# Performance work log

Hardware: AMD Instinct MI355X
Metric: run time of the kernel (lower is better)

## Reference

```python
import jax, jax.numpy as jnp
import numpy as np

BINS = 128
H, W = 4096, 4096


def setup_inputs() -> dict:
    key = jax.random.key(0)
    k1, k2 = jax.random.split(key)
    img = jax.random.randint(k1, (H, W, 3), 0, 256, dtype=jnp.int32)
    mask = jax.random.uniform(k2, (H, W), dtype=jnp.float32)
    full = jnp.zeros((BINS, BINS, BINS), dtype=jnp.float32)
    lines = jnp.zeros((BINS, BINS, BINS), dtype=jnp.float32)
    return {"img": img, "mask": mask, "full": full, "lines": lines}


def reference(img, mask, full, lines):
    # quantize 0..255 -> 0..127 (matches uint8 img // 2)
    q = (img // 2)[:, :, :3]
    h, w, _ = q.shape
    flat = q.reshape(h * w, 3)  # [N, 3] bin indices
    r, g, b = flat[:, 0], flat[:, 1], flat[:, 2]

    # _push_image: scatter-add into 128^3 histograms
    full2 = full.at[r, g, b].add(1.0)
    lines2 = lines.at[r, g, b].add(mask.reshape(h * w))

    # get_ratios: normalized log-likelihood-ratio threshold filter
    l = lines2 + 1e-10
    f = full2 + 1.0
    l = l / jnp.sum(l)
    f = f / jnp.sum(f)
    log_ratios = jnp.log(l / f)
    avg_log_ratios = jnp.sum(l * log_ratios)
    color_filter = log_ratios > avg_log_ratios  # [128,128,128] bool

    # _apply_filter: per-pixel gather from the 3D lookup table
    out = color_filter[q[..., 0], q[..., 1], q[..., 2]]  # [H, W] bool
    return out
```

## Files before the change

### kernel.cpp

```cpp
#include <hip/hip_runtime.h>
#include <stdint.h>


typedef uint32_t u32x4 __attribute__((ext_vector_type(4)));

#define P1_BLK    512
#define P1_PIXG   1024

#define NBKT_N    128
#define SHIFT_N   14
#define CAP_N     135168
#define NBKT_M    512
#define SHIFT_M   12
#define CAP_M     34816
#define BPB_M     4096

#define NSUB      32
#define SUBCAP    4608
#define NSEG      (NBKT_N * NSUB)
#define P15_SPLIT 8

template<int NB, int SHIFT, int CAPV, bool WBPIX>
__global__ __launch_bounds__(P1_BLK) void p1_scatter_det(
    const u32x4* __restrict__ img4, const u32x4* __restrict__ mask4,
    uint32_t* __restrict__ cursor,
    unsigned short* __restrict__ gbin, unsigned long long* __restrict__ gpm,
    u32x4* __restrict__ bpix4)
{
    __shared__ uint32_t s_cnt[NB];
    __shared__ uint32_t s_start[NB];
    __shared__ int      s_adj[NB];
    __shared__ uint32_t s_wsum[P1_BLK / 64];
    __shared__ uint32_t s_bin[P1_PIXG * 4];
    __shared__ unsigned long long s_pm[P1_PIXG * 4];

    const int tid = threadIdx.x;
    if (tid < NB) s_cnt[tid] = 0;
    __syncthreads();

    const int g0 = blockIdx.x * P1_PIXG;
    uint32_t bin[8], rk[8];
    unsigned long long pm[8];

    #pragma unroll
    for (int k = 0; k < 2; ++k) {
        int g = g0 + tid + k * P1_BLK;
        u32x4 a = __builtin_nontemporal_load(&img4[3 * g + 0]);
        u32x4 b = __builtin_nontemporal_load(&img4[3 * g + 1]);
        u32x4 c = __builtin_nontemporal_load(&img4[3 * g + 2]);
        u32x4 m = __builtin_nontemporal_load(&mask4[g]);
        uint32_t b0 = ((a.x >> 1) << 14) | ((a.y >> 1) << 7) | (a.z >> 1);
        uint32_t b1 = ((a.w >> 1) << 14) | ((b.x >> 1) << 7) | (b.y >> 1);
        uint32_t b2 = ((b.z >> 1) << 14) | ((b.w >> 1) << 7) | (c.x >> 1);
        uint32_t b3 = ((c.y >> 1) << 14) | ((c.z >> 1) << 7) | (c.w >> 1);
        if (WBPIX) {
            u32x4 bb = {b0, b1, b2, b3};
            __builtin_nontemporal_store(bb, &bpix4[g]);
        }
        unsigned long long p0 = (unsigned long long)(4u * (uint32_t)g);
        bin[4*k+0] = b0; pm[4*k+0] = ((p0 + 0) << 32) | m.x; rk[4*k+0] = atomicAdd(&s_cnt[b0 >> SHIFT], 1u);
        bin[4*k+1] = b1; pm[4*k+1] = ((p0 + 1) << 32) | m.y; rk[4*k+1] = atomicAdd(&s_cnt[b1 >> SHIFT], 1u);
        bin[4*k+2] = b2; pm[4*k+2] = ((p0 + 2) << 32) | m.z; rk[4*k+2] = atomicAdd(&s_cnt[b2 >> SHIFT], 1u);
        bin[4*k+3] = b3; pm[4*k+3] = ((p0 + 3) << 32) | m.w; rk[4*k+3] = atomicAdd(&s_cnt[b3 >> SHIFT], 1u);
    }
    __syncthreads();

    uint32_t v = (tid < NB) ? s_cnt[tid] : 0u;
    uint32_t inc = v;
    #pragma unroll
    for (int o = 1; o < 64; o <<= 1) {
        uint32_t n = __shfl_up(inc, o, 64);
        if ((tid & 63) >= o) inc += n;
    }
    if ((tid & 63) == 63) s_wsum[tid >> 6] = inc;
    __syncthreads();
    if (tid == 0) {
        uint32_t run = 0;
        #pragma unroll
        for (int w = 0; w < P1_BLK / 64; ++w) { uint32_t t = s_wsum[w]; s_wsum[w] = run; run += t; }
    }
    __syncthreads();
    uint32_t start = inc - v + s_wsum[tid >> 6];
    if (tid < NB) {
        s_start[tid] = start;
        uint32_t gb = v ? atomicAdd(&cursor[tid], v) : 0u;
        s_adj[tid] = (int)gb - (int)start;
    }
    __syncthreads();

    #pragma unroll
    for (int k = 0; k < 8; ++k) {
        uint32_t slot = s_start[bin[k] >> SHIFT] + rk[k];
        s_bin[slot] = bin[k];
        s_pm[slot]  = pm[k];
    }
    __syncthreads();

    for (int i = tid; i < P1_PIXG * 4; i += P1_BLK) {
        uint32_t bf = s_bin[i];
        uint32_t bk = bf >> SHIFT;
        uint32_t pos = (uint32_t)(s_adj[bk] + i);
        if (pos < (uint32_t)CAPV) {
            size_t idx = (size_t)bk * CAPV + pos;
            gbin[idx] = (unsigned short)(bf & ((1u << SHIFT) - 1u));
            gpm[idx]  = s_pm[i];
        }
    }
}

__global__ __launch_bounds__(1024) void p15_subpart(
    const unsigned short* __restrict__ gbin,
    const unsigned long long* __restrict__ gpm,
    const uint32_t* __restrict__ cursor,
    unsigned short* __restrict__ gb2,
    unsigned long long* __restrict__ gpm2,
    uint32_t* __restrict__ cnt2)
{
    __shared__ uint32_t s_c[NSUB], s_st[NSUB + 1], s_gp[NSUB];
    __shared__ unsigned short s_sb[4096];
    __shared__ unsigned long long s_sp[4096];

    const int tid  = threadIdx.x;
    const int b    = blockIdx.x >> 3;
    const int part = blockIdx.x & (P15_SPLIT - 1);
    uint32_t n = cursor[b];
    if (n > CAP_N) n = CAP_N;
    const size_t base = (size_t)b * CAP_N;

    for (uint32_t c0 = (uint32_t)part * 4096u; c0 < n; c0 += P15_SPLIT * 4096u) {
        const uint32_t cn = (n - c0 < 4096u) ? (n - c0) : 4096u;
        if (tid < NSUB) s_c[tid] = 0u;
        __syncthreads();

        uint32_t myb[4]; unsigned long long myp[4]; uint32_t myr[4];
        #pragma unroll
        for (int k = 0; k < 4; ++k) {
            uint32_t i = (uint32_t)tid + k * 1024u;
            if (i < cn) {
                uint32_t bl = gbin[base + c0 + i];
                myp[k] = gpm[base + c0 + i];
                myr[k] = atomicAdd(&s_c[bl >> 9], 1u);
                myb[k] = bl;
            } else myb[k] = 0xFFFFFFFFu;
        }
        __syncthreads();
        if (tid == 0) {
            uint32_t run = 0;
            #pragma unroll
            for (int r = 0; r < NSUB; ++r) { s_st[r] = run; run += s_c[r]; }
            s_st[NSUB] = run;
        }
        if (tid < NSUB) {
            uint32_t c = s_c[tid];
            s_gp[tid] = c ? atomicAdd(&cnt2[b * NSUB + tid], c) : 0u;
        }
        __syncthreads();
        #pragma unroll
        for (int k = 0; k < 4; ++k) {
            if (myb[k] != 0xFFFFFFFFu) {
                uint32_t slot = s_st[myb[k] >> 9] + myr[k];
                s_sb[slot] = (unsigned short)myb[k];
                s_sp[slot] = myp[k];
            }
        }
        __syncthreads();

        for (uint32_t i = tid; i < cn; i += 1024) {
            uint32_t bl = s_sb[i];
            uint32_t r = bl >> 9;
            uint32_t pos = s_gp[r] + (i - s_st[r]);
            if (pos < SUBCAP) {
                size_t d = ((size_t)b * NSUB + r) * SUBCAP + pos;
                gb2[d]  = (unsigned short)bl;
                gpm2[d] = s_sp[i];
            }
        }
        __syncthreads();
    }
}

__global__ __launch_bounds__(512) void p2_binhist(
    const unsigned short* __restrict__ gb2,
    const unsigned long long* __restrict__ gpm2,
    const uint32_t* __restrict__ cnt2,
    uint32_t* __restrict__ counts, float* __restrict__ lsum)
{
    __shared__ uint32_t s_cnt[512], s_start[512];
    __shared__ uint32_t s_wt[8];
    __shared__ unsigned long long s_srt[SUBCAP];

    const int tid = threadIdx.x;
    const int s = blockIdx.x;
    uint32_t n = cnt2[s];
    if (n > SUBCAP) n = SUBCAP;
    const size_t base = (size_t)s * SUBCAP;

    s_cnt[tid] = 0u;
    __syncthreads();

    uint32_t           myb[9];
    unsigned long long myp[9];
    uint32_t           myr[9];
    #pragma unroll
    for (int k = 0; k < 9; ++k) {
        uint32_t i = (uint32_t)tid + (uint32_t)k * 512u;
        if (i < n) {
            uint32_t lo = gb2[base + i] & 511u;
            myp[k] = gpm2[base + i];
            myr[k] = atomicAdd(&s_cnt[lo], 1u);
            myb[k] = lo;
        } else myb[k] = 0xFFFFFFFFu;
    }
    __syncthreads();

    uint32_t v = s_cnt[tid], inc = v;
    #pragma unroll
    for (int o = 1; o < 64; o <<= 1) {
        uint32_t t = __shfl_up(inc, o, 64);
        if ((tid & 63) >= o) inc += t;
    }
    if ((tid & 63) == 63) s_wt[tid >> 6] = inc;
    __syncthreads();
    if (tid == 0) {
        uint32_t run = 0;
        #pragma unroll
        for (int w = 0; w < 8; ++w) { uint32_t t = s_wt[w]; s_wt[w] = run; run += t; }
    }
    __syncthreads();
    const uint32_t st = s_wt[tid >> 6] + inc - v;
    s_start[tid] = st;
    __syncthreads();

    #pragma unroll
    for (int k = 0; k < 9; ++k) {
        if (myb[k] != 0xFFFFFFFFu)
            s_srt[s_start[myb[k]] + myr[k]] = myp[k];
    }
    __syncthreads();

    const uint32_t c = v;
    for (uint32_t x = 1; x < c; ++x) {
        unsigned long long val = s_srt[st + x];
        int y = (int)x - 1;
        while (y >= 0 && s_srt[st + y] > val) { s_srt[st + y + 1] = s_srt[st + y]; --y; }
        s_srt[st + y + 1] = val;
    }
    float sum = 0.0f;
    for (uint32_t x = 0; x < c; ++x)
        sum += __uint_as_float((uint32_t)s_srt[st + x]);
    counts[(size_t)s * 512 + tid] = c;
    lsum[(size_t)s * 512 + tid]   = sum;
}

__global__ __launch_bounds__(1024) void p2_sort_hist(
    const unsigned short* __restrict__ gbin,
    const unsigned long long* __restrict__ gpm,
    const uint32_t* __restrict__ cursor,
    unsigned long long* __restrict__ srt,
    uint32_t* __restrict__ counts, float* __restrict__ lsum)
{
    __shared__ uint32_t s_cnt[BPB_M];
    __shared__ uint32_t s_start[BPB_M];
    __shared__ uint32_t s_fill[BPB_M];
    __shared__ uint32_t s_wt[16];

    const int tid = threadIdx.x;
    const int b = blockIdx.x;
    for (int j = tid; j < BPB_M; j += 1024) s_cnt[j] = 0u;
    __syncthreads();

    uint32_t n = cursor[b];
    if (n > CAP_M) n = CAP_M;
    const size_t base = (size_t)b * CAP_M;

    for (uint32_t i = tid; i < n; i += 1024)
        atomicAdd(&s_cnt[gbin[base + i]], 1u);
    __syncthreads();

    const int j0 = tid * 4;
    uint32_t a0 = s_cnt[j0+0], a1 = s_cnt[j0+1], a2 = s_cnt[j0+2], a3 = s_cnt[j0+3];
    uint32_t s = a0 + a1 + a2 + a3;
    uint32_t inc = s;
    #pragma unroll
    for (int o = 1; o < 64; o <<= 1) {
        uint32_t t = __shfl_up(inc, o, 64);
        if ((tid & 63) >= o) inc += t;
    }
    if ((tid & 63) == 63) s_wt[tid >> 6] = inc;
    __syncthreads();
    if (tid == 0) {
        uint32_t run = 0;
        #pragma unroll
        for (int w = 0; w < 16; ++w) { uint32_t t = s_wt[w]; s_wt[w] = run; run += t; }
    }
    __syncthreads();
    uint32_t ex = s_wt[tid >> 6] + (inc - s);
    uint32_t e0 = ex, e1 = ex + a0, e2 = e1 + a1, e3 = e2 + a2;
    s_start[j0+0] = e0; s_start[j0+1] = e1; s_start[j0+2] = e2; s_start[j0+3] = e3;
    s_fill[j0+0] = 0u;  s_fill[j0+1] = 0u;  s_fill[j0+2] = 0u;  s_fill[j0+3] = 0u;
    __syncthreads();

    for (uint32_t i = tid; i < n; i += 1024) {
        uint32_t lo = gbin[base + i];
        unsigned long long pmv = __builtin_nontemporal_load(&gpm[base + i]);
        uint32_t slot = s_start[lo] + atomicAdd(&s_fill[lo], 1u);
        srt[base + slot] = pmv;
    }
    __threadfence_block();
    __syncthreads();

    uint32_t cs[4] = {a0, a1, a2, a3};
    uint32_t ss[4] = {e0, e1, e2, e3};
    #pragma unroll
    for (int t = 0; t < 4; ++t) {
        uint32_t c = cs[t];
        unsigned long long* arr = srt + base + ss[t];
        for (uint32_t x = 1; x < c; ++x) {
            unsigned long long v2 = arr[x];
            int y = (int)x - 1;
            while (y >= 0 && arr[y] > v2) { arr[y+1] = arr[y]; --y; }
            arr[y+1] = v2;
        }
        float sum = 0.0f;
        for (uint32_t x = 0; x < c; ++x)
            sum += __uint_as_float((uint32_t)arr[x]);
        size_t gbidx = (size_t)b * BPB_M + (size_t)(j0 + t);
        counts[gbidx] = c;
        lsum[gbidx]   = sum;
    }
}

__global__ void hist_direct_kernel(const u32x4* __restrict__ img4,
                                   const u32x4* __restrict__ mask4,
                                   uint32_t* __restrict__ counts,
                                   float* __restrict__ lsum, int npix4) {
    int t = blockIdx.x * blockDim.x + threadIdx.x;
    if (t >= npix4) return;
    u32x4 a = img4[3 * t + 0];
    u32x4 b = img4[3 * t + 1];
    u32x4 c = img4[3 * t + 2];
    u32x4 m = mask4[t];
    uint32_t b0 = ((a.x >> 1) << 14) | ((a.y >> 1) << 7) | (a.z >> 1);
    uint32_t b1 = ((a.w >> 1) << 14) | ((b.x >> 1) << 7) | (b.y >> 1);
    uint32_t b2 = ((b.z >> 1) << 14) | ((b.w >> 1) << 7) | (c.x >> 1);
    uint32_t b3 = ((c.y >> 1) << 14) | ((c.z >> 1) << 7) | (c.w >> 1);
    atomicAdd(&counts[b0], 1u);
    atomicAdd(&counts[b1], 1u);
    atomicAdd(&counts[b2], 1u);
    atomicAdd(&counts[b3], 1u);
    unsafeAtomicAdd(&lsum[b0], __uint_as_float(m.x));
    unsafeAtomicAdd(&lsum[b1], __uint_as_float(m.y));
    unsafeAtomicAdd(&lsum[b2], __uint_as_float(m.z));
    unsafeAtomicAdd(&lsum[b3], __uint_as_float(m.w));
}

__global__ __launch_bounds__(256) void reduce_lf_kernel(
    const uint32_t* __restrict__ counts, const float* __restrict__ lsum,
    const float* __restrict__ full_in, const float* __restrict__ lines_in,
    double* __restrict__ part_lf, int nbin) {
    double sl = 0.0, sf = 0.0;
    for (int i = blockIdx.x * 256 + threadIdx.x; i < nbin; i += 256 * 256) {
        float f = (float)counts[i] + full_in[i] + 1.0f;
        float l = (lsum[i] + lines_in[i]) + 1e-10f;
        sl += (double)l;
        sf += (double)f;
    }
    for (int o = 32; o > 0; o >>= 1) {
        sl += __shfl_down(sl, o, 64);
        sf += __shfl_down(sf, o, 64);
    }
    __shared__ double s0[4], s1[4];
    int lane = threadIdx.x & 63, wid = threadIdx.x >> 6;
    if (lane == 0) { s0[wid] = sl; s1[wid] = sf; }
    __syncthreads();
    if (threadIdx.x == 0) {
        part_lf[blockIdx.x * 2 + 0] = s0[0] + s0[1] + s0[2] + s0[3];
        part_lf[blockIdx.x * 2 + 1] = s1[0] + s1[1] + s1[2] + s1[3];
    }
}

__global__ void final_lf_kernel(const double* __restrict__ part_lf,
                                double* __restrict__ accum) {
    const int lane = threadIdx.x;
    double sl = 0.0, sf = 0.0;
    #pragma unroll
    for (int k = 0; k < 4; ++k) {
        sl += part_lf[2 * (lane + 64 * k) + 0];
        sf += part_lf[2 * (lane + 64 * k) + 1];
    }
    #pragma unroll
    for (int o = 32; o > 0; o >>= 1) {
        sl += __shfl_down(sl, o, 64);
        sf += __shfl_down(sf, o, 64);
    }
    if (lane == 0) { accum[0] = sl; accum[1] = sf; }
}

__global__ __launch_bounds__(256) void logr_kernel(
    const uint32_t* __restrict__ counts, const float* __restrict__ lsum,
    const float* __restrict__ full_in, const float* __restrict__ lines_in,
    const double* __restrict__ accum, double* __restrict__ part_avg,
    float* __restrict__ logr, int nbin) {
    float Sl = (float)accum[0];
    float Sf = (float)accum[1];
    double acc = 0.0;
    for (int i = blockIdx.x * 256 + threadIdx.x; i < nbin; i += 256 * 256) {
        float f = (float)counts[i] + full_in[i] + 1.0f;
        float l = (lsum[i] + lines_in[i]) + 1e-10f;
        float ln = l / Sl;
        float fn = f / Sf;
        float lr = logf(ln / fn);
        logr[i] = lr;
        acc += (double)(ln * lr);
    }
    for (int o = 32; o > 0; o >>= 1) acc += __shfl_down(acc, o, 64);
    __shared__ double s[4];
    int lane = threadIdx.x & 63, wid = threadIdx.x >> 6;
    if (lane == 0) s[wid] = acc;
    __syncthreads();
    if (threadIdx.x == 0) part_avg[blockIdx.x] = s[0] + s[1] + s[2] + s[3];
}

__global__ void final_avg_kernel(const double* __restrict__ part_avg,
                                 double* __restrict__ accum) {
    const int lane = threadIdx.x;
    double a = 0.0;
    #pragma unroll
    for (int k = 0; k < 4; ++k) a += part_avg[lane + 64 * k];
    #pragma unroll
    for (int o = 32; o > 0; o >>= 1) a += __shfl_down(a, o, 64);
    if (lane == 0) accum[2] = a;
}

__global__ void filt_kernel(const float* __restrict__ logr,
                            const double* __restrict__ accum,
                            unsigned long long* __restrict__ bits, int nbin) {
    float avg = (float)accum[2];
    int i = blockIdx.x * blockDim.x + threadIdx.x;
    bool p = (i < nbin) && (logr[i] > avg);
    unsigned long long m = __ballot(p);
    if ((threadIdx.x & 63) == 0 && i < nbin) bits[i >> 6] = m;
}

__global__ void out_kernel_bpix(const u32x4* __restrict__ bpix4,
                                const uint32_t* __restrict__ bits32,
                                u32x4* __restrict__ out4, int npix4) {
    int t = blockIdx.x * blockDim.x + threadIdx.x;
    if (t >= npix4) return;
    u32x4 b = __builtin_nontemporal_load(&bpix4[t]);
    u32x4 o = {(bits32[b.x >> 5] >> (b.x & 31u)) & 1u,
               (bits32[b.y >> 5] >> (b.y & 31u)) & 1u,
               (bits32[b.z >> 5] >> (b.z & 31u)) & 1u,
               (bits32[b.w >> 5] >> (b.w & 31u)) & 1u};
    __builtin_nontemporal_store(o, &out4[t]);
}

__global__ void out_kernel_img(const u32x4* __restrict__ img4,
                               const uint32_t* __restrict__ bits32,
                               u32x4* __restrict__ out4, int npix4) {
    int t = blockIdx.x * blockDim.x + threadIdx.x;
    if (t >= npix4) return;
    u32x4 a = __builtin_nontemporal_load(&img4[3 * t + 0]);
    u32x4 b = __builtin_nontemporal_load(&img4[3 * t + 1]);
    u32x4 c = __builtin_nontemporal_load(&img4[3 * t + 2]);
    uint32_t b0 = ((a.x >> 1) << 14) | ((a.y >> 1) << 7) | (a.z >> 1);
    uint32_t b1 = ((a.w >> 1) << 14) | ((b.x >> 1) << 7) | (b.y >> 1);
    uint32_t b2 = ((b.z >> 1) << 14) | ((b.w >> 1) << 7) | (c.x >> 1);
    uint32_t b3 = ((c.y >> 1) << 14) | ((c.z >> 1) << 7) | (c.w >> 1);
    u32x4 o = {(bits32[b0 >> 5] >> (b0 & 31u)) & 1u,
               (bits32[b1 >> 5] >> (b1 & 31u)) & 1u,
               (bits32[b2 >> 5] >> (b2 & 31u)) & 1u,
               (bits32[b3 >> 5] >> (b3 & 31u)) & 1u};
    __builtin_nontemporal_store(o, &out4[t]);
}

extern "C" void kernel_launch(void* const* d_in, const int* in_sizes, int n_in,
                              void* d_out, int out_size, void* d_ws, size_t ws_size,
                              hipStream_t stream) {
    const int*   img      = (const int*)d_in[0];
    const float* mask     = (const float*)d_in[1];
    const float* full_in  = (const float*)d_in[2];
    const float* lines_in = (const float*)d_in[3];

    const int npix  = in_sizes[1];
    const int nbin  = in_sizes[2];
    const int npix4 = npix / 4;

    char* ws = (char*)d_ws;
    const size_t ENT1 = (size_t)NBKT_M * CAP_M;
    const size_t ENT2 = (size_t)NSEG * SUBCAP;

    const size_t off_cursor = 64;
    const size_t off_plf    = off_cursor + 4ull * NBKT_M;
    const size_t off_pavg   = off_plf + 256ull * 2 * 8;
    const size_t off_cnt2   = off_pavg + 256ull * 8;
    const size_t off_hdrend = (off_cnt2 + 4ull * NSEG + 255ull) & ~255ull;
    const size_t off_counts = off_hdrend;
    const size_t off_lsum   = off_counts + 4ull * nbin;
    const size_t off_logr   = off_lsum + 4ull * nbin;
    const size_t off_filt   = off_logr + 4ull * nbin;
    const size_t off_gbin   = (off_filt + (size_t)nbin + 255ull) & ~255ull;
    const size_t off_gpm    = (off_gbin + 2ull * ENT1 + 255ull) & ~255ull;
    const size_t off_union  = off_gpm + 8ull * ENT1;
    const size_t need_mid   = off_union + 8ull * ENT1;
    const size_t off_gb2    = off_union;
    const size_t off_gpm2   = (off_gb2 + 2ull * ENT2 + 255ull) & ~255ull;
    const size_t need_new   = off_gpm2 + 8ull * ENT2;
    const size_t off_bpix   = (need_new + 255ull) & ~255ull;
    const size_t need_new2  = off_bpix + 4ull * (size_t)npix;

    double*   accum  = (double*)ws;
    uint32_t* cursor = (uint32_t*)(ws + off_cursor);
    double*   plf    = (double*)(ws + off_plf);
    double*   pavg   = (double*)(ws + off_pavg);
    uint32_t* cnt2   = (uint32_t*)(ws + off_cnt2);
    uint32_t* counts = (uint32_t*)(ws + off_counts);
    float*    lsum   = (float*)(ws + off_lsum);
    float*    logr   = (float*)(ws + off_logr);
    unsigned long long* fbits = (unsigned long long*)(ws + off_filt);
    const uint32_t*     fb32  = (const uint32_t*)(ws + off_filt);
    unsigned short*     gbin = (unsigned short*)(ws + off_gbin);
    unsigned long long* gpm  = (unsigned long long*)(ws + off_gpm);
    unsigned long long* srt  = (unsigned long long*)(ws + off_union);
    unsigned short*     gb2  = (unsigned short*)(ws + off_gb2);
    unsigned long long* gpm2 = (unsigned long long*)(ws + off_gpm2);
    u32x4*              bpix4 = (u32x4*)(ws + off_bpix);

    const bool shape_ok  = (nbin == NBKT_M * BPB_M) && (npix % (P1_PIXG * 4) == 0);
    const bool tier_new2 = shape_ok && ws_size >= need_new2;
    const bool tier_new  = shape_ok && ws_size >= need_new;
    const bool tier_mid  = shape_ok && ws_size >= need_mid;
    const int BLK = 256;

    if (tier_new2 || tier_new) {
        hipMemsetAsync(ws, 0, off_hdrend, stream);
        if (tier_new2) {
            p1_scatter_det<NBKT_N, SHIFT_N, CAP_N, true>
                <<<npix / (P1_PIXG * 4), P1_BLK, 0, stream>>>(
                (const u32x4*)img, (const u32x4*)mask, cursor, gbin, gpm, bpix4);
        } else {
            p1_scatter_det<NBKT_N, SHIFT_N, CAP_N, false>
                <<<npix / (P1_PIXG * 4), P1_BLK, 0, stream>>>(
                (const u32x4*)img, (const u32x4*)mask, cursor, gbin, gpm, nullptr);
        }
        p15_subpart<<<NBKT_N * P15_SPLIT, 1024, 0, stream>>>(
            gbin, gpm, cursor, gb2, gpm2, cnt2);
        p2_binhist<<<NSEG, 512, 0, stream>>>(gb2, gpm2, cnt2, counts, lsum);
    } else if (tier_mid) {
        hipMemsetAsync(ws, 0, off_hdrend, stream);
        p1_scatter_det<NBKT_M, SHIFT_M, CAP_M, false>
            <<<npix / (P1_PIXG * 4), P1_BLK, 0, stream>>>(
            (const u32x4*)img, (const u32x4*)mask, cursor, gbin, gpm, nullptr);
        p2_sort_hist<<<NBKT_M, 1024, 0, stream>>>(gbin, gpm, cursor, srt, counts, lsum);
    } else {
        hipMemsetAsync(ws, 0, off_logr, stream);
        hist_direct_kernel<<<(npix4 + BLK - 1) / BLK, BLK, 0, stream>>>(
            (const u32x4*)img, (const u32x4*)mask, counts, lsum, npix4);
    }

    reduce_lf_kernel<<<256, 256, 0, stream>>>(counts, lsum, full_in, lines_in, plf, nbin);
    final_lf_kernel<<<1, 64, 0, stream>>>(plf, accum);
    logr_kernel<<<256, 256, 0, stream>>>(counts, lsum, full_in, lines_in,
                                         accum, pavg, logr, nbin);
    final_avg_kernel<<<1, 64, 0, stream>>>(pavg, accum);
    filt_kernel<<<(nbin + BLK - 1) / BLK, BLK, 0, stream>>>(logr, accum, fbits, nbin);
    if (tier_new2) {
        out_kernel_bpix<<<(npix4 + BLK - 1) / BLK, BLK, 0, stream>>>(
            bpix4, fb32, (u32x4*)d_out, npix4);
    } else {
        out_kernel_img<<<(npix4 + BLK - 1) / BLK, BLK, 0, stream>>>(
            (const u32x4*)img, fb32, (u32x4*)d_out, npix4);
    }
}
```

Before: 690.0 us.

## Pack bin into 64-bit payload, fuse histogram finalize with l/f sum reduction

Drops the separate 16-bit bin array between the subpartition and per-bin histogram stages by packing the low bin bits, pixel index and 31-bit mask into one 64-bit word. The scatter stage stores a compact per-slot metadata word plus mask in shared memory instead of a 64-bit payload. The histogram kernel now computes the final f and l values and per-block partial sums directly, so the separate reduce pass over counts and lsum goes away. The cost is extra bit packing, a new constraint on pixel count, and extra fA/lA buffers.

```diff
diff --git a/kernel.cpp b/kernel.cpp
--- a/kernel.cpp
+++ b/kernel.cpp
@@ -20,27 +20,27 @@
 #define NSEG      (NBKT_N * NSUB)
 #define P15_SPLIT 8
 
-template<int NB, int SHIFT, int CAPV, bool WBPIX>
-__global__ __launch_bounds__(P1_BLK) void p1_scatter_det(
+template<bool WBPIX>
+__global__ __launch_bounds__(P1_BLK) void p1_scatter_new(
     const u32x4* __restrict__ img4, const u32x4* __restrict__ mask4,
     uint32_t* __restrict__ cursor,
     unsigned short* __restrict__ gbin, unsigned long long* __restrict__ gpm,
     u32x4* __restrict__ bpix4)
 {
-    __shared__ uint32_t s_cnt[NB];
-    __shared__ uint32_t s_start[NB];
-    __shared__ int      s_adj[NB];
+    __shared__ uint32_t s_cnt[NBKT_N];
+    __shared__ uint32_t s_start[NBKT_N];
+    __shared__ int      s_adj[NBKT_N];
     __shared__ uint32_t s_wsum[P1_BLK / 64];
-    __shared__ uint32_t s_bin[P1_PIXG * 4];
-    __shared__ unsigned long long s_pm[P1_PIXG * 4];
+    __shared__ uint32_t s_meta[P1_PIXG * 4];
+    __shared__ uint32_t s_msk[P1_PIXG * 4];
+    __shared__ uint8_t  s_bkt[P1_PIXG * 4];
 
     const int tid = threadIdx.x;
-    if (tid < NB) s_cnt[tid] = 0;
+    if (tid < NBKT_N) s_cnt[tid] = 0;
     __syncthreads();
 
     const int g0 = blockIdx.x * P1_PIXG;
-    uint32_t bin[8], rk[8];
-    unsigned long long pm[8];
+    uint32_t bin[8], rk[8], msk[8];
 
     #pragma unroll
     for (int k = 0; k < 2; ++k) {
@@ -57,6 +57,93 @@
             u32x4 bb = {b0, b1, b2, b3};
             __builtin_nontemporal_store(bb, &bpix4[g]);
         }
+        bin[4*k+0] = b0; msk[4*k+0] = m.x; rk[4*k+0] = atomicAdd(&s_cnt[b0 >> SHIFT_N], 1u);
+        bin[4*k+1] = b1; msk[4*k+1] = m.y; rk[4*k+1] = atomicAdd(&s_cnt[b1 >> SHIFT_N], 1u);
+        bin[4*k+2] = b2; msk[4*k+2] = m.z; rk[4*k+2] = atomicAdd(&s_cnt[b2 >> SHIFT_N], 1u);
+        bin[4*k+3] = b3; msk[4*k+3] = m.w; rk[4*k+3] = atomicAdd(&s_cnt[b3 >> SHIFT_N], 1u);
+    }
+    __syncthreads();
+
+    uint32_t v = (tid < NBKT_N) ? s_cnt[tid] : 0u;
+    uint32_t inc = v;
+    #pragma unroll
+    for (int o = 1; o < 64; o <<= 1) {
+        uint32_t n = __shfl_up(inc, o, 64);
+        if ((tid & 63) >= o) inc += n;
+    }
+    if ((tid & 63) == 63) s_wsum[tid >> 6] = inc;
+    __syncthreads();
+    if (tid == 0) {
+        uint32_t run = 0;
+        #pragma unroll
+        for (int w = 0; w < P1_BLK / 64; ++w) { uint32_t t = s_wsum[w]; s_wsum[w] = run; run += t; }
+    }
+    __syncthreads();
+    uint32_t start = inc - v + s_wsum[tid >> 6];
+    if (tid < NBKT_N) {
+        s_start[tid] = start;
+        uint32_t gb = v ? atomicAdd(&cursor[tid], v) : 0u;
+        s_adj[tid] = (int)gb - (int)start;
+    }
+    __syncthreads();
+
+    #pragma unroll
+    for (int k = 0; k < 8; ++k) {
+        uint32_t slot = s_start[bin[k] >> SHIFT_N] + rk[k];
+        s_meta[slot] = (bin[k] & 0x3FFFu) | ((uint32_t)tid << 14) | ((uint32_t)k << 23);
+        s_msk[slot]  = msk[k];
+        s_bkt[slot]  = (uint8_t)(bin[k] >> SHIFT_N);
+    }
+    __syncthreads();
+
+    for (int i = tid; i < P1_PIXG * 4; i += P1_BLK) {
+        uint32_t m  = s_meta[i];
+        uint32_t bk = s_bkt[i];
+        uint32_t pos = (uint32_t)(s_adj[bk] + i);
+        if (pos < (uint32_t)CAP_N) {
+            size_t idx = (size_t)bk * CAP_N + pos;
+            uint32_t t9 = (m >> 14) & 511u;
+            uint32_t kk = m >> 23;
+            uint32_t g  = (uint32_t)g0 + t9 + (kk >> 2) * P1_BLK;
+            uint32_t pix = 4u * g + (kk & 3u);
+            gbin[idx] = (unsigned short)(m & 0x3FFFu);
+            gpm[idx]  = ((unsigned long long)pix << 32) | (unsigned long long)s_msk[i];
+        }
+    }
+}
+
+template<int NB, int SHIFT, int CAPV>
+__global__ __launch_bounds__(P1_BLK) void p1_scatter_det(
+    const u32x4* __restrict__ img4, const u32x4* __restrict__ mask4,
+    uint32_t* __restrict__ cursor,
+    unsigned short* __restrict__ gbin, unsigned long long* __restrict__ gpm)
+{
+    __shared__ uint32_t s_cnt[NB];
+    __shared__ uint32_t s_start[NB];
+    __shared__ int      s_adj[NB];
+    __shared__ uint32_t s_wsum[P1_BLK / 64];
+    __shared__ uint32_t s_bin[P1_PIXG * 4];
+    __shared__ unsigned long long s_pm[P1_PIXG * 4];
+
+    const int tid = threadIdx.x;
+    if (tid < NB) s_cnt[tid] = 0;
+    __syncthreads();
+
+    const int g0 = blockIdx.x * P1_PIXG;
+    uint32_t bin[8], rk[8];
+    unsigned long long pm[8];
+
+    #pragma unroll
+    for (int k = 0; k < 2; ++k) {
+        int g = g0 + tid + k * P1_BLK;
+        u32x4 a = __builtin_nontemporal_load(&img4[3 * g + 0]);
+        u32x4 b = __builtin_nontemporal_load(&img4[3 * g + 1]);
+        u32x4 c = __builtin_nontemporal_load(&img4[3 * g + 2]);
+        u32x4 m = __builtin_nontemporal_load(&mask4[g]);
+        uint32_t b0 = ((a.x >> 1) << 14) | ((a.y >> 1) << 7) | (a.z >> 1);
+        uint32_t b1 = ((a.w >> 1) << 14) | ((b.x >> 1) << 7) | (b.y >> 1);
+        uint32_t b2 = ((b.z >> 1) << 14) | ((b.w >> 1) << 7) | (c.x >> 1);
+        uint32_t b3 = ((c.y >> 1) << 14) | ((c.z >> 1) << 7) | (c.w >> 1);
         unsigned long long p0 = (unsigned long long)(4u * (uint32_t)g);
         bin[4*k+0] = b0; pm[4*k+0] = ((p0 + 0) << 32) | m.x; rk[4*k+0] = atomicAdd(&s_cnt[b0 >> SHIFT], 1u);
         bin[4*k+1] = b1; pm[4*k+1] = ((p0 + 1) << 32) | m.y; rk[4*k+1] = atomicAdd(&s_cnt[b1 >> SHIFT], 1u);
@@ -112,13 +199,12 @@
     const unsigned short* __restrict__ gbin,
     const unsigned long long* __restrict__ gpm,
     const uint32_t* __restrict__ cursor,
-    unsigned short* __restrict__ gb2,
     unsigned long long* __restrict__ gpm2,
     uint32_t* __restrict__ cnt2)
 {
     __shared__ uint32_t s_c[NSUB], s_st[NSUB + 1], s_gp[NSUB];
-    __shared__ unsigned short s_sb[4096];
     __shared__ unsigned long long s_sp[4096];
+    __shared__ uint8_t s_sub[4096];
 
     const int tid  = threadIdx.x;
     const int b    = blockIdx.x >> 3;
@@ -132,16 +218,19 @@
         if (tid < NSUB) s_c[tid] = 0u;
         __syncthreads();
 
-        uint32_t myb[4]; unsigned long long myp[4]; uint32_t myr[4];
+        uint32_t sub[4]; unsigned long long pk[4]; uint32_t myr[4];
         #pragma unroll
         for (int k = 0; k < 4; ++k) {
             uint32_t i = (uint32_t)tid + k * 1024u;
             if (i < cn) {
                 uint32_t bl = gbin[base + c0 + i];
-                myp[k] = gpm[base + c0 + i];
-                myr[k] = atomicAdd(&s_c[bl >> 9], 1u);
-                myb[k] = bl;
-            } else myb[k] = 0xFFFFFFFFu;
+                unsigned long long pm = gpm[base + c0 + i];
+                pk[k] = ((unsigned long long)(bl & 511u) << 55)
+                      | ((pm >> 32) << 31)
+                      | (pm & 0x7FFFFFFFull);
+                sub[k] = bl >> 9;
+                myr[k] = atomicAdd(&s_c[sub[k]], 1u);
+            } else sub[k] = 0xFFFFFFFFu;
         }
         __syncthreads();
         if (tid == 0) {
@@ -157,21 +246,19 @@
         __syncthreads();
         #pragma unroll
         for (int k = 0; k < 4; ++k) {
-            if (myb[k] != 0xFFFFFFFFu) {
-                uint32_t slot = s_st[myb[k] >> 9] + myr[k];
-                s_sb[slot] = (unsigned short)myb[k];
-                s_sp[slot] = myp[k];
+            if (sub[k] != 0xFFFFFFFFu) {
+                uint32_t slot = s_st[sub[k]] + myr[k];
+                s_sp[slot]  = pk[k];
+                s_sub[slot] = (uint8_t)sub[k];
             }
         }
         __syncthreads();
 
         for (uint32_t i = tid; i < cn; i += 1024) {
-            uint32_t bl = s_sb[i];
-            uint32_t r = bl >> 9;
+            uint32_t r = s_sub[i];
             uint32_t pos = s_gp[r] + (i - s_st[r]);
             if (pos < SUBCAP) {
                 size_t d = ((size_t)b * NSUB + r) * SUBCAP + pos;
-                gb2[d]  = (unsigned short)bl;
                 gpm2[d] = s_sp[i];
             }
         }
@@ -180,14 +267,17 @@
 }
 
 __global__ __launch_bounds__(512) void p2_binhist(
-    const unsigned short* __restrict__ gb2,
     const unsigned long long* __restrict__ gpm2,
     const uint32_t* __restrict__ cnt2,
-    uint32_t* __restrict__ counts, float* __restrict__ lsum)
+    const float* __restrict__ full_in, const float* __restrict__ lines_in,
+    float* __restrict__ fA, float* __restrict__ lA,
+    double* __restrict__ plf)
 {
-    __shared__ uint32_t s_cnt[512], s_start[512];
+    __shared__ uint32_t s_cnt[512];
+    __shared__ unsigned short s_start[512];
     __shared__ uint32_t s_wt[8];
     __shared__ unsigned long long s_srt[SUBCAP];
+    __shared__ double s_d0[8], s_d1[8];
 
     const int tid = threadIdx.x;
     const int s = blockIdx.x;
@@ -205,8 +295,9 @@
     for (int k = 0; k < 9; ++k) {
         uint32_t i = (uint32_t)tid + (uint32_t)k * 512u;
         if (i < n) {
-            uint32_t lo = gb2[base + i] & 511u;
-            myp[k] = gpm2[base + i];
+            unsigned long long pv = gpm2[base + i];
+            uint32_t lo = (uint32_t)(pv >> 55);
+            myp[k] = pv;
             myr[k] = atomicAdd(&s_cnt[lo], 1u);
             myb[k] = lo;
         } else myb[k] = 0xFFFFFFFFu;
@@ -228,13 +319,13 @@
     }
     __syncthreads();
     const uint32_t st = s_wt[tid >> 6] + inc - v;
-    s_start[tid] = st;
+    s_start[tid] = (unsigned short)st;
     __syncthreads();
 
     #pragma unroll
     for (int k = 0; k < 9; ++k) {
         if (myb[k] != 0xFFFFFFFFu)
-            s_srt[s_start[myb[k]] + myr[k]] = myp[k];
+            s_srt[(uint32_t)s_start[myb[k]] + myr[k]] = myp[k];
     }
     __syncthreads();
 
@@ -247,9 +338,30 @@
     }
     float sum = 0.0f;
     for (uint32_t x = 0; x < c; ++x)
-        sum += __uint_as_float((uint32_t)s_srt[st + x]);
-    counts[(size_t)s * 512 + tid] = c;
-    lsum[(size_t)s * 512 + tid]   = sum;
+        sum += __uint_as_float((uint32_t)s_srt[st + x] & 0x7FFFFFFFu);
+
+    const size_t gb = (size_t)s * 512 + tid;
+    float f = (float)c + full_in[gb] + 1.0f;
+    float l = (sum + lines_in[gb]) + 1e-10f;
+    fA[gb] = f;
+    lA[gb] = l;
+
+    double sl = (double)l, sf = (double)f;
+    #pragma unroll
+    for (int o = 32; o > 0; o >>= 1) {
+        sl += __shfl_down(sl, o, 64);
+        sf += __shfl_down(sf, o, 64);
+    }
+    const int lane = tid & 63, wid = tid >> 6;
+    if (lane == 0) { s_d0[wid] = sl; s_d1[wid] = sf; }
+    __syncthreads();
+    if (tid == 0) {
+        double a0 = 0.0, a1 = 0.0;
+        #pragma unroll
+        for (int w = 0; w < 8; ++w) { a0 += s_d0[w]; a1 += s_d1[w]; }
+        plf[2 * s + 0] = a0;
+        plf[2 * s + 1] = a1;
+    }
 }
 
 __global__ __launch_bounds__(1024) void p2_sort_hist(
@@ -354,59 +466,73 @@
     unsafeAtomicAdd(&lsum[b3], __uint_as_float(m.w));
 }
 
-__global__ __launch_bounds__(256) void reduce_lf_kernel(
+__global__ __launch_bounds__(512) void fuse_fl_kernel(
     const uint32_t* __restrict__ counts, const float* __restrict__ lsum,
     const float* __restrict__ full_in, const float* __restrict__ lines_in,
-    double* __restrict__ part_lf, int nbin) {
-    double sl = 0.0, sf = 0.0;
-    for (int i = blockIdx.x * 256 + threadIdx.x; i < nbin; i += 256 * 256) {
-        float f = (float)counts[i] + full_in[i] + 1.0f;
-        float l = (lsum[i] + lines_in[i]) + 1e-10f;
-        sl += (double)l;
-        sf += (double)f;
-    }
+    float* __restrict__ fA, float* __restrict__ lA,
+    double* __restrict__ plf)
+{
+    __shared__ double s_d0[8], s_d1[8];
+    const int tid = threadIdx.x;
+    const int s = blockIdx.x;
+    const size_t gb = (size_t)s * 512 + tid;
+    float f = (float)counts[gb] + full_in[gb] + 1.0f;
+    float l = (lsum[gb] + lines_in[gb]) + 1e-10f;
+    fA[gb] = f;
+    lA[gb] = l;
+    double sl = (double)l, sf = (double)f;
+    #pragma unroll
     for (int o = 32; o > 0; o >>= 1) {
         sl += __shfl_down(sl, o, 64);
         sf += __shfl_down(sf, o, 64);
     }
+    const int lane = tid & 63, wid = tid >> 6;
+    if (lane == 0) { s_d0[wid] = sl; s_d1[wid] = sf; }
+    __syncthreads();
+    if (tid == 0) {
+        double a0 = 0.0, a1 = 0.0;
+        #pragma unroll
+        for (int w = 0; w < 8; ++w) { a0 += s_d0[w]; a1 += s_d1[w]; }
+        plf[2 * s + 0] = a0;
+        plf[2 * s + 1] = a1;
+    }
+}
+
+__global__ __launch_bounds__(256) void final_lf_kernel(
+    const double* __restrict__ plf, double* __restrict__ accum) {
     __shared__ double s0[4], s1[4];
-    int lane = threadIdx.x & 63, wid = threadIdx.x >> 6;
-    if (lane == 0) { s0[wid] = sl; s1[wid] = sf; }
-    __syncthreads();
-    if (threadIdx.x == 0) {
-        part_lf[blockIdx.x * 2 + 0] = s0[0] + s0[1] + s0[2] + s0[3];
-        part_lf[blockIdx.x * 2 + 1] = s1[0] + s1[1] + s1[2] + s1[3];
-    }
-}
-
-__global__ void final_lf_kernel(const double* __restrict__ part_lf,
-                                double* __restrict__ accum) {
-    const int lane = threadIdx.x;
+    const int tid = threadIdx.x;
     double sl = 0.0, sf = 0.0;
     #pragma unroll
-    for (int k = 0; k < 4; ++k) {
-        sl += part_lf[2 * (lane + 64 * k) + 0];
-        sf += part_lf[2 * (lane + 64 * k) + 1];
+    for (int k = 0; k < NSEG / 256; ++k) {
+        int j = tid + 256 * k;
+        sl += plf[2 * j + 0];
+        sf += plf[2 * j + 1];
     }
     #pragma unroll
     for (int o = 32; o > 0; o >>= 1) {
         sl += __shfl_down(sl, o, 64);
         sf += __shfl_down(sf, o, 64);
     }
-    if (lane == 0) { accum[0] = sl; accum[1] = sf; }
+    const int lane = tid & 63, wid = tid >> 6;
+    if (lane == 0) { s0[wid] = sl; s1[wid] = sf; }
+    __syncthreads();
+    if (tid == 0) {
+        accum[0] = s0[0] + s0[1] + s0[2] + s0[3];
+        accum[1] = s1[0] + s1[1] + s1[2] + s1[3];
+    }
 }
 
 __global__ __launch_bounds__(256) void logr_kernel(
-    const uint32_t* __restrict__ counts, const float* __restrict__ lsum,
-    const float* __restrict__ full_in, const float* __restrict__ lines_in,
+    const float* __restrict__ fA, const float* __restrict__ lA,
     const double* __restrict__ accum, double* __restrict__ part_avg,
     float* __restrict__ logr, int nbin) {
     float Sl = (float)accum[0];
     float Sf = (float)accum[1];
     double acc = 0.0;
     for (int i = blockIdx.x * 256 + threadIdx.x; i < nbin; i += 256 * 256) {
-        float f = (float)counts[i] + full_in[i] + 1.0f;
-        float l = (lsum[i] + lines_in[i]) + 1e-10f;
+        float f = fA[i];
+        float l = lA[i];
         float ln = l / Sl;
         float fn = f / Sf;
         float lr = logf(ln / fn);
@@ -492,19 +618,20 @@
 
     const size_t off_cursor = 64;
     const size_t off_plf    = off_cursor + 4ull * NBKT_M;
-    const size_t off_pavg   = off_plf + 256ull * 2 * 8;
+    const size_t off_pavg   = off_plf + 2ull * NSEG * 8;
     const size_t off_cnt2   = off_pavg + 256ull * 8;
     const size_t off_hdrend = (off_cnt2 + 4ull * NSEG + 255ull) & ~255ull;
     const size_t off_counts = off_hdrend;
     const size_t off_lsum   = off_counts + 4ull * nbin;
-    const size_t off_logr   = off_lsum + 4ull * nbin;
+    const size_t off_fA     = off_lsum + 4ull * nbin;
+    const size_t off_lA     = off_fA + 4ull * nbin;
+    const size_t off_logr   = off_lA + 4ull * nbin;
     const size_t off_filt   = off_logr + 4ull * nbin;
     const size_t off_gbin   = (off_filt + (size_t)nbin + 255ull) & ~255ull;
     const size_t off_gpm    = (off_gbin + 2ull * ENT1 + 255ull) & ~255ull;
     const size_t off_union  = off_gpm + 8ull * ENT1;
     const size_t need_mid   = off_union + 8ull * ENT1;
-    const size_t off_gb2    = off_union;
-    const size_t off_gpm2   = (off_gb2 + 2ull * ENT2 + 255ull) & ~255ull;
+    const size_t off_gpm2   = off_union;
     const size_t need_new   = off_gpm2 + 8ull * ENT2;
     const size_t off_bpix   = (need_new + 255ull) & ~255ull;
     const size_t need_new2  = off_bpix + 4ull * (size_t)npix;
@@ -516,52 +643,56 @@
     uint32_t* cnt2   = (uint32_t*)(ws + off_cnt2);
     uint32_t* counts = (uint32_t*)(ws + off_counts);
     float*    lsum   = (float*)(ws + off_lsum);
+    float*    fA     = (float*)(ws + off_fA);
+    float*    lA     = (float*)(ws + off_lA);
     float*    logr   = (float*)(ws + off_logr);
     unsigned long long* fbits = (unsigned long long*)(ws + off_filt);
     const uint32_t*     fb32  = (const uint32_t*)(ws + off_filt);
     unsigned short*     gbin = (unsigned short*)(ws + off_gbin);
     unsigned long long* gpm  = (unsigned long long*)(ws + off_gpm);
     unsigned long long* srt  = (unsigned long long*)(ws + off_union);
-    unsigned short*     gb2  = (unsigned short*)(ws + off_gb2);
     unsigned long long* gpm2 = (unsigned long long*)(ws + off_gpm2);
     u32x4*              bpix4 = (u32x4*)(ws + off_bpix);
 
     const bool shape_ok  = (nbin == NBKT_M * BPB_M) && (npix % (P1_PIXG * 4) == 0);
-    const bool tier_new2 = shape_ok && ws_size >= need_new2;
-    const bool tier_new  = shape_ok && ws_size >= need_new;
+    const bool pack_ok   = shape_ok && (npix <= (1 << 24));
+    const bool tier_new2 = pack_ok && ws_size >= need_new2;
+    const bool tier_new  = pack_ok && ws_size >= need_new;
     const bool tier_mid  = shape_ok && ws_size >= need_mid;
     const int BLK = 256;
 
     if (tier_new2 || tier_new) {
         hipMemsetAsync(ws, 0, off_hdrend, stream);
         if (tier_new2) {
-            p1_scatter_det<NBKT_N, SHIFT_N, CAP_N, true>
-                <<<npix / (P1_PIXG * 4), P1_BLK, 0, stream>>>(
+            p1_scatter_new<true><<<npix / (P1_PIXG * 4), P1_BLK, 0, stream>>>(
                 (const u32x4*)img, (const u32x4*)mask, cursor, gbin, gpm, bpix4);
         } else {
-            p1_scatter_det<NBKT_N, SHIFT_N, CAP_N, false>
-                <<<npix / (P1_PIXG * 4), P1_BLK, 0, stream>>>(
+            p1_scatter_new<false><<<npix / (P1_PIXG * 4), P1_BLK, 0, stream>>>(
                 (const u32x4*)img, (const u32x4*)mask, cursor, gbin, gpm, nullptr);
         }
         p15_subpart<<<NBKT_N * P15_SPLIT, 1024, 0, stream>>>(
-            gbin, gpm, cursor, gb2, gpm2, cnt2);
-        p2_binhist<<<NSEG, 512, 0, stream>>>(gb2, gpm2, cnt2, counts, lsum);
+            gbin, gpm, cursor, gpm2, cnt2);
+        p2_binhist<<<NSEG, 512, 0, stream>>>(gpm2, cnt2, full_in, lines_in,
+                                             fA, lA, plf);
     } else if (tier_mid) {
         hipMemsetAsync(ws, 0, off_hdrend, stream);
-        p1_scatter_det<NBKT_M, SHIFT_M, CAP_M, false>
+        p1_scatter_det<NBKT_M, SHIFT_M, CAP_M>
             <<<npix / (P1_PIXG * 4), P1_BLK, 0, stream>>>(
-            (const u32x4*)img, (const u32x4*)mask, cursor, gbin, gpm, nullptr);
+            (const u32x4*)img, (const u32x4*)mask, cursor, gbin, gpm);
         p2_sort_hist<<<NBKT_M, 1024, 0, stream>>>(gbin, gpm, cursor, srt, counts, lsum);
+        fuse_fl_kernel<<<NSEG, 512, 0, stream>>>(counts, lsum, full_in, lines_in,
+                                                 fA, lA, plf);
     } else {
-        hipMemsetAsync(ws, 0, off_logr, stream);
+        hipMemsetAsync(ws, 0, off_hdrend, stream);
+        hipMemsetAsync(ws + off_counts, 0, 8ull * nbin, stream);
         hist_direct_kernel<<<(npix4 + BLK - 1) / BLK, BLK, 0, stream>>>(
             (const u32x4*)img, (const u32x4*)mask, counts, lsum, npix4);
-    }
-
-    reduce_lf_kernel<<<256, 256, 0, stream>>>(counts, lsum, full_in, lines_in, plf, nbin);
-    final_lf_kernel<<<1, 64, 0, stream>>>(plf, accum);
-    logr_kernel<<<256, 256, 0, stream>>>(counts, lsum, full_in, lines_in,
-                                         accum, pavg, logr, nbin);
+        fuse_fl_kernel<<<NSEG, 512, 0, stream>>>(counts, lsum, full_in, lines_in,
+                                                 fA, lA, plf);
+    }
+
+    final_lf_kernel<<<1, 256, 0, stream>>>(plf, accum);
+    logr_kernel<<<256, 256, 0, stream>>>(fA, lA, accum, pavg, logr, nbin);
     final_avg_kernel<<<1, 64, 0, stream>>>(pavg, accum);
     filt_kernel<<<(nbin + BLK - 1) / BLK, BLK, 0, stream>>>(logr, accum, fbits, nbin);
     if (tier_new2) {
```

Measured after the change: 649.8 us. 1.06x faster.
